# Kernel tuning notes

Hardware: AMD Instinct MI355X
Metric: run time of the kernel (lower is better)

## Reference

```python
import jax, jax.numpy as jnp
import numpy as np

B = 2048
IN = 1024
M = 256
P = M * (M + 1) // 2  # 32896 Cholesky params


def setup_inputs() -> dict:
    key = jax.random.key(0)
    k1, k2, k3 = jax.random.split(key, 3)
    x = jax.random.normal(k1, (B, IN), dtype=jnp.float32)
    # nn.Linear(input_size, P): weight [P, IN], bias [P]
    bound = 1.0 / np.sqrt(IN)
    W = jax.random.uniform(k2, (P, IN), dtype=jnp.float32, minval=-bound, maxval=bound)
    b = jax.random.uniform(k3, (P,), dtype=jnp.float32, minval=-bound, maxval=bound)
    return {"x": x, "W": W, "b": b}


def reference(x, W, b):
    # Linear projection to packed lower-triangular params [B, P]
    chol_params = x @ W.T + b
    # Row-major lower-triangular fill order matches the torch double loop:
    # (0,0),(1,0),(1,1),(2,0),...
    rows, cols = jnp.tril_indices(M)
    diag_mask = rows == cols  # [P]
    vals = jnp.where(diag_mask[None, :], jax.nn.relu(chol_params), chol_params)
    L = jnp.zeros((x.shape[0], M, M), dtype=chol_params.dtype)
    L = L.at[:, rows, cols].set(vals)
    # Batched L @ L^T -> positive semi-definite matrix [B, M, M]
    return jnp.einsum('bik,bjk->bij', L, L)
```

## Files before the change

kernel.cpp:

```cpp
#include <hip/hip_runtime.h>

#define B_DIM 2048
#define IN_DIM 1024
#define M_DIM 256
#define P_DIM 32896
#define RTP_B 40960
#define CRTP_BYTES (167772160)
#define WQ_BYTES   (33685504)
#define XQ_BYTES   (2097152)

typedef __attribute__((ext_vector_type(4)))  int   i32x4;
typedef __attribute__((ext_vector_type(4)))  float f32x4;
typedef __attribute__((ext_vector_type(8)))  short short8;

#define GLD16(gsrc, ldst) __builtin_amdgcn_global_load_lds(                    \
    (const __attribute__((address_space(1))) unsigned int*)(gsrc),             \
    (__attribute__((address_space(3))) unsigned int*)(ldst), 16, 0, 0)

__device__ __forceinline__ unsigned short f2bf(float f) {
    unsigned int u = __float_as_uint(f);
    u += 0x7FFFu + ((u >> 16) & 1u);
    return (unsigned short)(u >> 16);
}
__device__ __forceinline__ int rtp0(int r) {
    const int g = r >> 6;
    return 2048 * g * (g + 1) + (r & 63) * ((g + 1) << 6);
}
__device__ __forceinline__ int rtp_off(int r, int c) {
    return rtp0(r) + (((c >> 3) ^ (r & 7)) << 3) + (c & 7);
}

#define NW_BLK 8224
#define NX_BLK 512
#define NZ_BLK 2048
__global__ void prep_all(const float* __restrict__ X, const float* __restrict__ W,
                         signed char* __restrict__ Xq, signed char* __restrict__ Wq,
                         float* __restrict__ Sx, unsigned short* __restrict__ Crtp) {
    const int bid = blockIdx.x, tid = threadIdx.x;
    if (bid < NW_BLK) {
#pragma unroll
        for (int u = 0; u < 4; ++u) {
            const int i = bid * 1024 + u * 256 + tid;
            float4 v = reinterpret_cast<const float4*>(W)[i];
            const int q0 = (int)rintf(v.x * 4064.f), q1 = (int)rintf(v.y * 4064.f);
            const int q2 = (int)rintf(v.z * 4064.f), q3 = (int)rintf(v.w * 4064.f);
            reinterpret_cast<unsigned int*>(Wq)[i] =
                (q0 & 255) | ((q1 & 255) << 8) | ((q2 & 255) << 16) | ((unsigned)(q3 & 255) << 24);
        }
    } else if (bid < NW_BLK + NX_BLK) {
        const int wv  = tid >> 6, ln = tid & 63;
        const int row = (bid - NW_BLK) * 4 + wv;
        const float* xr = X + (size_t)row * IN_DIM + ln * 16;
        float f[16];
#pragma unroll
        for (int u = 0; u < 4; ++u) {
            float4 v = reinterpret_cast<const float4*>(xr)[u];
            f[u * 4 + 0] = v.x; f[u * 4 + 1] = v.y; f[u * 4 + 2] = v.z; f[u * 4 + 3] = v.w;
        }
        float m = 0.f;
#pragma unroll
        for (int e = 0; e < 16; ++e) m = fmaxf(m, fabsf(f[e]));
#pragma unroll
        for (int off = 1; off < 64; off <<= 1) m = fmaxf(m, __shfl_xor(m, off));
        const float inv = m > 1e-30f ? 127.f / m : 0.f;
        unsigned int w4[4];
#pragma unroll
        for (int u = 0; u < 4; ++u) {
            const int q0 = (int)rintf(f[u * 4 + 0] * inv), q1 = (int)rintf(f[u * 4 + 1] * inv);
            const int q2 = (int)rintf(f[u * 4 + 2] * inv), q3 = (int)rintf(f[u * 4 + 3] * inv);
            w4[u] = (q0 & 255) | ((q1 & 255) << 8) | ((q2 & 255) << 16) | ((unsigned)(q3 & 255) << 24);
        }
        reinterpret_cast<uint4*>(Xq + (size_t)row * IN_DIM)[ln] =
            make_uint4(w4[0], w4[1], w4[2], w4[3]);
        if (ln == 0) Sx[row] = m / (127.f * 4064.f);
    } else {
        const int b = bid - NW_BLK - NX_BLK;
        const int r = tid;
        const int g = r >> 6;
        const int nch = (g + 1) << 3;
        const int xm = r & 7;
        unsigned short* base = Crtp + (size_t)b * RTP_B + rtp0(r);
        const int pc = (r >> 3) ^ xm;
        for (int c = r + 1; (c >> 3) == (r >> 3); ++c) base[(pc << 3) + (c & 7)] = 0;
        const uint4 z = make_uint4(0u, 0u, 0u, 0u);
        for (int cc = (r >> 3) + 1; cc < nch; ++cc)
            *reinterpret_cast<uint4*>(&base[(cc ^ xm) << 3]) = z;
    }
}

__global__ __launch_bounds__(512) void gemm1_kernel(
    const signed char* __restrict__ Xq, const signed char* __restrict__ Wq,
    const float* __restrict__ bias, const float* __restrict__ Sx,
    unsigned short* __restrict__ Crtp)
{
    __shared__ __align__(16) unsigned char lds[3 * 24576];

    const int lin = blockIdx.x;
    const int x   = lin & 7;
    const int j   = lin >> 3;
    const int rtile = ((x & 1) << 2) + (j & 3);
    const int panel = (x >> 1) * 65 + (j >> 2);
    if (panel >= 257) return;
    const int row0 = rtile << 8;
    const int col0 = panel << 7;

    const int tid  = threadIdx.x;
    const int lane = tid & 63;
    const int wid  = tid >> 6;
    const int wr   = wid >> 1;
    const int wc   = wid & 1;
    const int lr16 = lane & 15;
    const int kq   = lane >> 4;

    const int srow = lane >> 2;
    const int sch  = lane & 3;
    const signed char* gA = Xq + (size_t)(row0 + (wid << 5) + srow) * IN_DIM + (sch << 4);
    const signed char* gB = Wq + (size_t)(col0 + (wid << 4) + srow) * IN_DIM + (sch << 4);

#define STAGE(kt, bufo)                                                          \
    {                                                                            \
        GLD16(gA + ((kt) << 6),                        &lds[(bufo) + (wid << 11)]); \
        GLD16(gA + (size_t)16 * IN_DIM + ((kt) << 6),  &lds[(bufo) + (wid << 11) + 1024]); \
        GLD16(gB + ((kt) << 6),                        &lds[(bufo) + 16384 + (wid << 10)]); \
    }

    i32x4 acc[4][4];
#pragma unroll
    for (int m = 0; m < 4; ++m)
#pragma unroll
        for (int n = 0; n < 4; ++n) acc[m][n] = (i32x4){0, 0, 0, 0};

    int o0 = 0, o1 = 24576, o2 = 49152;
    STAGE(0, o0);
    STAGE(1, o1);

    for (int it = 0; it < 16; ++it) {
        if (it < 15) asm volatile("s_waitcnt vmcnt(3)" ::: "memory");
        else         asm volatile("s_waitcnt vmcnt(0)" ::: "memory");
        __builtin_amdgcn_s_barrier();
        asm volatile("" ::: "memory");

        const int cb = o0;
        i32x4 av[4], bv[4];
#pragma unroll
        for (int m = 0; m < 4; ++m) {
            const int r = (wr << 6) + (m << 4) + lr16;
            av[m] = *reinterpret_cast<const i32x4*>(&lds[cb + (r << 6) + (kq << 4)]);
        }
#pragma unroll
        for (int n = 0; n < 4; ++n) {
            const int r = (wc << 6) + (n << 4) + lr16;
            bv[n] = *reinterpret_cast<const i32x4*>(&lds[cb + 16384 + (r << 6) + (kq << 4)]);
        }
        if (it < 14) STAGE(it + 2, o2);
        __builtin_amdgcn_s_setprio(1);
#pragma unroll
        for (int m = 0; m < 4; ++m)
#pragma unroll
            for (int n = 0; n < 4; ++n)
                acc[m][n] = __builtin_amdgcn_mfma_i32_16x16x64_i8(av[m], bv[n], acc[m][n], 0, 0, 0);
        __builtin_amdgcn_s_setprio(0);

        const int t = o0; o0 = o1; o1 = o2; o2 = t;
    }
#undef STAGE

    float sc[4][4];
#pragma unroll
    for (int m = 0; m < 4; ++m)
#pragma unroll
        for (int q = 0; q < 4; ++q)
            sc[m][q] = Sx[row0 + (wr << 6) + (m << 4) + (kq << 2) + q];

#pragma unroll
    for (int n = 0; n < 4; ++n) {
        const int p = col0 + (wc << 6) + (n << 4) + lr16;
        const float t = sqrtf((float)(8 * p + 1));
        const int rt = (int)((t - 1.0f) * 0.5f + 0.001f);
        const int ct = p - ((rt * (rt + 1)) >> 1);
        const int off = rtp_off(rt, ct);
        const bool diag = (ct == rt);
        const float bvs = bias[p];
#pragma unroll
        for (int m = 0; m < 4; ++m) {
#pragma unroll
            for (int q = 0; q < 4; ++q) {
                const int brow = row0 + (wr << 6) + (m << 4) + (kq << 2) + q;
                float v = (float)acc[m][n][q] * sc[m][q] + bvs;
                if (diag) v = fmaxf(v, 0.f);
                Crtp[(size_t)brow * RTP_B + off] = f2bf(v);
            }
        }
    }
}

__global__ __launch_bounds__(512) void syrk_kernel(
    const unsigned short* __restrict__ Crtp, float* __restrict__ O)
{
    __shared__ unsigned short Lt[RTP_B];
    const int tid  = threadIdx.x;
    const int lane = tid & 63;
    const int wid  = tid >> 6;
    const int b    = blockIdx.x;
    const unsigned short* Cb = Crtp + (size_t)b * RTP_B;

#pragma unroll
    for (int i = 0; i < 10; ++i) {
        const int g = wid * 10 + i;
        GLD16(Cb + g * 512 + (lane << 3), &Lt[g * 512]);
    }
    __syncthreads();

    const int lr16 = lane & 15;
    const int kc   = lane >> 4;
    float* Ob = O + (size_t)b * (M_DIM * M_DIM);

    const unsigned char LIST[8][3] = {
        {0x33, 0x00, 0x00},
        {0x22, 0x00, 0x00},
        {0x23, 0x01, 0x00},
        {0x32, 0x02, 0x00},
        {0x11, 0x12, 0x00},
        {0x21, 0x13, 0x00},
        {0x31, 0x10, 0x20},
        {0x30, 0x03, 0x00}};
    const int CNT[8] = {1, 2, 2, 2, 2, 2, 3, 2};
    const int cnt = CNT[wid];

    for (int tt = 0; tt < cnt; ++tt) {
        const int code = LIST[wid][tt];
        const int ti = code >> 4, tj = code & 15;

        int baseA[4], xA[4], baseB[4], xB[4];
#pragma unroll
        for (int m = 0; m < 4; ++m) {
            const int ia = (ti << 6) + (m << 4) + lr16;
            const int jb = (tj << 6) + (m << 4) + lr16;
            baseA[m] = rtp0(ia); xA[m] = ia & 7;
            baseB[m] = rtp0(jb); xB[m] = jb & 7;
        }
        f32x4 acc[4][4];
#pragma unroll
        for (int m = 0; m < 4; ++m)
#pragma unroll
            for (int n = 0; n < 4; ++n) acc[m][n] = (f32x4){0.f, 0.f, 0.f, 0.f};

        const int kmax = ti < tj ? ti : tj;
        for (int kt = 0; kt <= kmax; ++kt) {
#pragma unroll
            for (int s = 0; s < 2; ++s) {
                const int cidx = (kt << 3) + (s << 2) + kc;
                short8 a[4], bb[4];
#pragma unroll
                for (int m = 0; m < 4; ++m)
                    a[m] = *reinterpret_cast<const short8*>(&Lt[baseA[m] + ((cidx ^ xA[m]) << 3)]);
#pragma unroll
                for (int n = 0; n < 4; ++n)
                    bb[n] = *reinterpret_cast<const short8*>(&Lt[baseB[n] + ((cidx ^ xB[n]) << 3)]);
#pragma unroll
                for (int m = 0; m < 4; ++m)
#pragma unroll
                    for (int n = 0; n < 4; ++n)
                        acc[m][n] = __builtin_amdgcn_mfma_f32_16x16x32_bf16(a[m], bb[n], acc[m][n], 0, 0, 0);
            }
        }
#pragma unroll
        for (int m = 0; m < 4; ++m) {
            const int i0 = (ti << 6) + (m << 4) + (kc << 2);
#pragma unroll
            for (int n = 0; n < 4; ++n) {
                const int j = (tj << 6) + (n << 4) + lr16;
#pragma unroll
                for (int q = 0; q < 4; ++q)
                    __builtin_nontemporal_store(acc[m][n][q], &Ob[(size_t)(i0 + q) * M_DIM + j]);
            }
        }
    }
}

extern "C" void kernel_launch(void* const* d_in, const int* in_sizes, int n_in,
                              void* d_out, int out_size, void* d_ws, size_t ws_size,
                              hipStream_t stream)
{
    (void)in_sizes; (void)n_in; (void)out_size; (void)ws_size;
    const float* x    = (const float*)d_in[0];
    const float* W    = (const float*)d_in[1];
    const float* bias = (const float*)d_in[2];
    float* O = (float*)d_out;

    char* ws = (char*)d_ws;
    unsigned short* Crtp = (unsigned short*)ws;
    signed char*    Wq   = (signed char*)(ws + CRTP_BYTES);
    signed char*    Xq   = (signed char*)(ws + CRTP_BYTES + WQ_BYTES);
    float*          Sx   = (float*)(ws + CRTP_BYTES + WQ_BYTES + XQ_BYTES);

    prep_all<<<dim3(NW_BLK + NX_BLK + NZ_BLK), dim3(256), 0, stream>>>(
        x, W, Xq, Wq, Sx, Crtp);
    gemm1_kernel<<<dim3(2080), dim3(512), 0, stream>>>(Xq, Wq, bias, Sx, Crtp);
    syrk_kernel<<<dim3(B_DIM), dim3(512), 0, stream>>>(Crtp, O);
}
```

Before: 333.5 us.

## Split SYRK LDS load into two phases and compute early tiles during second load

The syrk kernel now loads the first 24 chunks of the packed L rows (covering rows 0-127) with a partial vmcnt wait and barrier. Two waves compute the tiles that depend only on those rows (00, 01, 10, 11) while the remaining chunks are still arriving. The other tiles are redistributed across waves after a second barrier. This overlaps global-to-LDS loading with MFMA work and the output stores, at the cost of less even per-wave work balance and reliance on hand-counted vmcnt values.

Measured after the change: 332.1 us. No clear change (-0.4%).

```diff
diff --git a/kernel.cpp b/kernel.cpp
--- a/kernel.cpp
+++ b/kernel.cpp
@@ -194,6 +194,56 @@
     }
 }
 
+__device__ __forceinline__ void syrk_tile(int code, const unsigned short* Lt,
+                                          float* __restrict__ Ob, int lr16, int kc)
+{
+    const int ti = code >> 4, tj = code & 15;
+    int baseA[4], xA[4], baseB[4], xB[4];
+#pragma unroll
+    for (int m = 0; m < 4; ++m) {
+        const int ia = (ti << 6) + (m << 4) + lr16;
+        const int jb = (tj << 6) + (m << 4) + lr16;
+        baseA[m] = rtp0(ia); xA[m] = ia & 7;
+        baseB[m] = rtp0(jb); xB[m] = jb & 7;
+    }
+    f32x4 acc[4][4];
+#pragma unroll
+    for (int m = 0; m < 4; ++m)
+#pragma unroll
+        for (int n = 0; n < 4; ++n) acc[m][n] = (f32x4){0.f, 0.f, 0.f, 0.f};
+
+    const int kmax = ti < tj ? ti : tj;
+    for (int kt = 0; kt <= kmax; ++kt) {
+#pragma unroll
+        for (int s = 0; s < 2; ++s) {
+            const int cidx = (kt << 3) + (s << 2) + kc;
+            short8 a[4], bb[4];
+#pragma unroll
+            for (int m = 0; m < 4; ++m)
+                a[m] = *reinterpret_cast<const short8*>(&Lt[baseA[m] + ((cidx ^ xA[m]) << 3)]);
+#pragma unroll
+            for (int n = 0; n < 4; ++n)
+                bb[n] = *reinterpret_cast<const short8*>(&Lt[baseB[n] + ((cidx ^ xB[n]) << 3)]);
+#pragma unroll
+            for (int m = 0; m < 4; ++m)
+#pragma unroll
+                for (int n = 0; n < 4; ++n)
+                    acc[m][n] = __builtin_amdgcn_mfma_f32_16x16x32_bf16(a[m], bb[n], acc[m][n], 0, 0, 0);
+        }
+    }
+#pragma unroll
+    for (int m = 0; m < 4; ++m) {
+        const int i0 = (ti << 6) + (m << 4) + (kc << 2);
+#pragma unroll
+        for (int n = 0; n < 4; ++n) {
+            const int j = (tj << 6) + (n << 4) + lr16;
+#pragma unroll
+            for (int q = 0; q < 4; ++q)
+                __builtin_nontemporal_store(acc[m][n][q], &Ob[(size_t)(i0 + q) * M_DIM + j]);
+        }
+    }
+}
+
 __global__ __launch_bounds__(512) void syrk_kernel(
     const unsigned short* __restrict__ Crtp, float* __restrict__ O)
 {
@@ -205,77 +255,47 @@
     const unsigned short* Cb = Crtp + (size_t)b * RTP_B;
 
 #pragma unroll
-    for (int i = 0; i < 10; ++i) {
-        const int g = wid * 10 + i;
+    for (int i = 0; i < 3; ++i) {
+        const int g = wid * 3 + i;
         GLD16(Cb + g * 512 + (lane << 3), &Lt[g * 512]);
     }
-    __syncthreads();
+#pragma unroll
+    for (int i = 0; i < 7; ++i) {
+        const int g = 24 + wid * 7 + i;
+        GLD16(Cb + g * 512 + (lane << 3), &Lt[g * 512]);
+    }
+    asm volatile("s_waitcnt vmcnt(7)" ::: "memory");
+    __builtin_amdgcn_s_barrier();
+    asm volatile("" ::: "memory");
 
     const int lr16 = lane & 15;
     const int kc   = lane >> 4;
     float* Ob = O + (size_t)b * (M_DIM * M_DIM);
 
-    const unsigned char LIST[8][3] = {
-        {0x33, 0x00, 0x00},
-        {0x22, 0x00, 0x00},
-        {0x23, 0x01, 0x00},
-        {0x32, 0x02, 0x00},
-        {0x11, 0x12, 0x00},
-        {0x21, 0x13, 0x00},
-        {0x31, 0x10, 0x20},
-        {0x30, 0x03, 0x00}};
-    const int CNT[8] = {1, 2, 2, 2, 2, 2, 3, 2};
-    const int cnt = CNT[wid];
-
-    for (int tt = 0; tt < cnt; ++tt) {
-        const int code = LIST[wid][tt];
-        const int ti = code >> 4, tj = code & 15;
-
-        int baseA[4], xA[4], baseB[4], xB[4];
-#pragma unroll
-        for (int m = 0; m < 4; ++m) {
-            const int ia = (ti << 6) + (m << 4) + lr16;
-            const int jb = (tj << 6) + (m << 4) + lr16;
-            baseA[m] = rtp0(ia); xA[m] = ia & 7;
-            baseB[m] = rtp0(jb); xB[m] = jb & 7;
-        }
-        f32x4 acc[4][4];
-#pragma unroll
-        for (int m = 0; m < 4; ++m)
-#pragma unroll
-            for (int n = 0; n < 4; ++n) acc[m][n] = (f32x4){0.f, 0.f, 0.f, 0.f};
-
-        const int kmax = ti < tj ? ti : tj;
-        for (int kt = 0; kt <= kmax; ++kt) {
-#pragma unroll
-            for (int s = 0; s < 2; ++s) {
-                const int cidx = (kt << 3) + (s << 2) + kc;
-                short8 a[4], bb[4];
-#pragma unroll
-                for (int m = 0; m < 4; ++m)
-                    a[m] = *reinterpret_cast<const short8*>(&Lt[baseA[m] + ((cidx ^ xA[m]) << 3)]);
-#pragma unroll
-                for (int n = 0; n < 4; ++n)
-                    bb[n] = *reinterpret_cast<const short8*>(&Lt[baseB[n] + ((cidx ^ xB[n]) << 3)]);
-#pragma unroll
-                for (int m = 0; m < 4; ++m)
-#pragma unroll
-                    for (int n = 0; n < 4; ++n)
-                        acc[m][n] = __builtin_amdgcn_mfma_f32_16x16x32_bf16(a[m], bb[n], acc[m][n], 0, 0, 0);
-            }
-        }
-#pragma unroll
-        for (int m = 0; m < 4; ++m) {
-            const int i0 = (ti << 6) + (m << 4) + (kc << 2);
-#pragma unroll
-            for (int n = 0; n < 4; ++n) {
-                const int j = (tj << 6) + (n << 4) + lr16;
-#pragma unroll
-                for (int q = 0; q < 4; ++q)
-                    __builtin_nontemporal_store(acc[m][n][q], &Ob[(size_t)(i0 + q) * M_DIM + j]);
-            }
-        }
-    }
+    const unsigned char L1[8][3] = {
+        {0,0,0},{0,0,0},{0,0,0},{0,0,0},{0,0,0},{0,0,0},
+        {0x11, 0, 0},
+        {0x00, 0x01, 0x10}};
+    const int C1[8] = {0, 0, 0, 0, 0, 0, 1, 3};
+    for (int tt = 0; tt < C1[wid]; ++tt)
+        syrk_tile(L1[wid][tt], Lt, Ob, lr16, kc);
+
+    asm volatile("s_waitcnt vmcnt(0)" ::: "memory");
+    __builtin_amdgcn_s_barrier();
+    asm volatile("" ::: "memory");
+
+    const unsigned char L2[8][2] = {
+        {0x33, 0x33},
+        {0x22, 0x02},
+        {0x23, 0x20},
+        {0x32, 0x30},
+        {0x12, 0x21},
+        {0x13, 0x31},
+        {0x03, 0x03},
+        {0x00, 0x00}};
+    const int C2[8] = {1, 2, 2, 2, 2, 2, 1, 0};
+    for (int tt = 0; tt < C2[wid]; ++tt)
+        syrk_tile(L2[wid][tt], Lt, Ob, lr16, kc);
 }
 
 extern "C" void kernel_launch(void* const* d_in, const int* in_sizes, int n_in,
```

## Enlarge int8 GEMM tiles to 256x256 and handle tail columns with separate blocks

Applied to the files above, without the earlier changes.

The main int8 GEMM moves from 256x128 tiles to 256x256 tiles, with eight waves each computing a 128x64 sub-tile, and LDS grows to three 32 KB buffers. The 128 leftover columns past 32768 are handled by extra blocks that load directly from global memory into MFMA without LDS. This doubles per-block data reuse and removes the swizzled 2080-block grid. The cost is more accumulator registers, lower occupancy from the larger LDS, and a slower unstaged tail path.

After: 351.2 us. 1.05x slower.

```diff
diff --git a/kernel.cpp b/kernel.cpp
--- a/kernel.cpp
+++ b/kernel.cpp
@@ -93,88 +93,31 @@
     const float* __restrict__ bias, const float* __restrict__ Sx,
     unsigned short* __restrict__ Crtp)
 {
-    __shared__ __align__(16) unsigned char lds[3 * 24576];
-
-    const int lin = blockIdx.x;
-    const int x   = lin & 7;
-    const int j   = lin >> 3;
-    const int rtile = ((x & 1) << 2) + (j & 3);
-    const int panel = (x >> 1) * 65 + (j >> 2);
-    if (panel >= 257) return;
-    const int row0 = rtile << 8;
-    const int col0 = panel << 7;
-
+    __shared__ __align__(16) unsigned char lds[3 * 32768];
+
+    const int bid  = blockIdx.x;
     const int tid  = threadIdx.x;
     const int lane = tid & 63;
     const int wid  = tid >> 6;
-    const int wr   = wid >> 1;
-    const int wc   = wid & 1;
     const int lr16 = lane & 15;
     const int kq   = lane >> 4;
 
-    const int srow = lane >> 2;
-    const int sch  = lane & 3;
-    const signed char* gA = Xq + (size_t)(row0 + (wid << 5) + srow) * IN_DIM + (sch << 4);
-    const signed char* gB = Wq + (size_t)(col0 + (wid << 4) + srow) * IN_DIM + (sch << 4);
-
-#define STAGE(kt, bufo)                                                          \
-    {                                                                            \
-        GLD16(gA + ((kt) << 6),                        &lds[(bufo) + (wid << 11)]); \
-        GLD16(gA + (size_t)16 * IN_DIM + ((kt) << 6),  &lds[(bufo) + (wid << 11) + 1024]); \
-        GLD16(gB + ((kt) << 6),                        &lds[(bufo) + 16384 + (wid << 10)]); \
-    }
-
-    i32x4 acc[4][4];
-#pragma unroll
-    for (int m = 0; m < 4; ++m)
-#pragma unroll
-        for (int n = 0; n < 4; ++n) acc[m][n] = (i32x4){0, 0, 0, 0};
-
-    int o0 = 0, o1 = 24576, o2 = 49152;
-    STAGE(0, o0);
-    STAGE(1, o1);
-
-    for (int it = 0; it < 16; ++it) {
-        if (it < 15) asm volatile("s_waitcnt vmcnt(3)" ::: "memory");
-        else         asm volatile("s_waitcnt vmcnt(0)" ::: "memory");
-        __builtin_amdgcn_s_barrier();
-        asm volatile("" ::: "memory");
-
-        const int cb = o0;
-        i32x4 av[4], bv[4];
-#pragma unroll
-        for (int m = 0; m < 4; ++m) {
-            const int r = (wr << 6) + (m << 4) + lr16;
-            av[m] = *reinterpret_cast<const i32x4*>(&lds[cb + (r << 6) + (kq << 4)]);
-        }
-#pragma unroll
-        for (int n = 0; n < 4; ++n) {
-            const int r = (wc << 6) + (n << 4) + lr16;
-            bv[n] = *reinterpret_cast<const i32x4*>(&lds[cb + 16384 + (r << 6) + (kq << 4)]);
-        }
-        if (it < 14) STAGE(it + 2, o2);
-        __builtin_amdgcn_s_setprio(1);
-#pragma unroll
-        for (int m = 0; m < 4; ++m)
-#pragma unroll
-            for (int n = 0; n < 4; ++n)
-                acc[m][n] = __builtin_amdgcn_mfma_i32_16x16x64_i8(av[m], bv[n], acc[m][n], 0, 0, 0);
-        __builtin_amdgcn_s_setprio(0);
-
-        const int t = o0; o0 = o1; o1 = o2; o2 = t;
-    }
-#undef STAGE
-
-    float sc[4][4];
-#pragma unroll
-    for (int m = 0; m < 4; ++m)
-#pragma unroll
-        for (int q = 0; q < 4; ++q)
-            sc[m][q] = Sx[row0 + (wr << 6) + (m << 4) + (kq << 2) + q];
-
-#pragma unroll
-    for (int n = 0; n < 4; ++n) {
-        const int p = col0 + (wc << 6) + (n << 4) + lr16;
+    if (bid >= 1024) {
+        const int tb = bid - 1024;
+        const int r0 = tb << 5;
+        i32x4 acc0 = (i32x4){0,0,0,0}, acc1 = (i32x4){0,0,0,0};
+        const signed char* pa0 = Xq + (size_t)(r0 + lr16) * IN_DIM + (kq << 4);
+        const signed char* pa1 = pa0 + 16 * IN_DIM;
+        const int p = 32768 + (wid << 4) + lr16;
+        const signed char* pb = Wq + (size_t)p * IN_DIM + (kq << 4);
+#pragma unroll 4
+        for (int s = 0; s < 16; ++s) {
+            i32x4 a0 = *reinterpret_cast<const i32x4*>(pa0 + (s << 6));
+            i32x4 a1 = *reinterpret_cast<const i32x4*>(pa1 + (s << 6));
+            i32x4 b0 = *reinterpret_cast<const i32x4*>(pb + (s << 6));
+            acc0 = __builtin_amdgcn_mfma_i32_16x16x64_i8(a0, b0, acc0, 0, 0, 0);
+            acc1 = __builtin_amdgcn_mfma_i32_16x16x64_i8(a1, b0, acc1, 0, 0, 0);
+        }
         const float t = sqrtf((float)(8 * p + 1));
         const int rt = (int)((t - 1.0f) * 0.5f + 0.001f);
         const int ct = p - ((rt * (rt + 1)) >> 1);
@@ -182,10 +125,101 @@
         const bool diag = (ct == rt);
         const float bvs = bias[p];
 #pragma unroll
-        for (int m = 0; m < 4; ++m) {
+        for (int m = 0; m < 2; ++m) {
+            const i32x4 a = m ? acc1 : acc0;
 #pragma unroll
             for (int q = 0; q < 4; ++q) {
-                const int brow = row0 + (wr << 6) + (m << 4) + (kq << 2) + q;
+                const int brow = r0 + (m << 4) + (kq << 2) + q;
+                float v = (float)a[q] * Sx[brow] + bvs;
+                if (diag) v = fmaxf(v, 0.f);
+                Crtp[(size_t)brow * RTP_B + off] = f2bf(v);
+            }
+        }
+        return;
+    }
+
+    const int row0 = (bid & 7) << 8;
+    const int col0 = (bid >> 3) << 8;
+    const int wr   = wid >> 2;
+    const int wn   = wid & 3;
+
+    const int srow = lane >> 2;
+    const int sch  = lane & 3;
+    const signed char* gA0 = Xq + (size_t)(row0 + (wid << 5) + srow) * IN_DIM + (sch << 4);
+    const signed char* gA1 = gA0 + (size_t)16 * IN_DIM;
+    const signed char* gB0 = Wq + (size_t)(col0 + (wid << 5) + srow) * IN_DIM + (sch << 4);
+    const signed char* gB1 = gB0 + (size_t)16 * IN_DIM;
+
+#define STAGE(kt, bufo)                                                        \
+    {                                                                          \
+        GLD16(gA0 + ((kt) << 6), &lds[(bufo) + (wid << 11)]);                  \
+        GLD16(gA1 + ((kt) << 6), &lds[(bufo) + (wid << 11) + 1024]);           \
+        GLD16(gB0 + ((kt) << 6), &lds[(bufo) + 16384 + (wid << 11)]);          \
+        GLD16(gB1 + ((kt) << 6), &lds[(bufo) + 16384 + (wid << 11) + 1024]);   \
+    }
+
+    i32x4 acc[8][4];
+#pragma unroll
+    for (int m = 0; m < 8; ++m)
+#pragma unroll
+        for (int n = 0; n < 4; ++n) acc[m][n] = (i32x4){0, 0, 0, 0};
+
+    int o0 = 0, o1 = 32768, o2 = 65536;
+    STAGE(0, o0);
+    STAGE(1, o1);
+
+    for (int it = 0; it < 16; ++it) {
+        if (it < 15) asm volatile("s_waitcnt vmcnt(4)" ::: "memory");
+        else         asm volatile("s_waitcnt vmcnt(0)" ::: "memory");
+        __builtin_amdgcn_s_barrier();
+        asm volatile("" ::: "memory");
+
+        const int cb = o0;
+        i32x4 av[8], bv[4];
+#pragma unroll
+        for (int m = 0; m < 8; ++m) {
+            const int r = (wr << 7) + (m << 4) + lr16;
+            av[m] = *reinterpret_cast<const i32x4*>(&lds[cb + (r << 6) + (kq << 4)]);
+        }
+#pragma unroll
+        for (int n = 0; n < 4; ++n) {
+            const int r = (wn << 6) + (n << 4) + lr16;
+            bv[n] = *reinterpret_cast<const i32x4*>(&lds[cb + 16384 + (r << 6) + (kq << 4)]);
+        }
+        if (it < 14) STAGE(it + 2, o2);
+        __builtin_amdgcn_s_setprio(1);
+#pragma unroll
+        for (int m = 0; m < 8; ++m)
+#pragma unroll
+            for (int n = 0; n < 4; ++n)
+                acc[m][n] = __builtin_amdgcn_mfma_i32_16x16x64_i8(av[m], bv[n], acc[m][n], 0, 0, 0);
+        __builtin_amdgcn_s_setprio(0);
+
+        const int t = o0; o0 = o1; o1 = o2; o2 = t;
+    }
+#undef STAGE
+
+    float sc[8][4];
+#pragma unroll
+    for (int m = 0; m < 8; ++m)
+#pragma unroll
+        for (int q = 0; q < 4; ++q)
+            sc[m][q] = Sx[row0 + (wr << 7) + (m << 4) + (kq << 2) + q];
+
+#pragma unroll
+    for (int n = 0; n < 4; ++n) {
+        const int p = col0 + (wn << 6) + (n << 4) + lr16;
+        const float t = sqrtf((float)(8 * p + 1));
+        const int rt = (int)((t - 1.0f) * 0.5f + 0.001f);
+        const int ct = p - ((rt * (rt + 1)) >> 1);
+        const int off = rtp_off(rt, ct);
+        const bool diag = (ct == rt);
+        const float bvs = bias[p];
+#pragma unroll
+        for (int m = 0; m < 8; ++m) {
+#pragma unroll
+            for (int q = 0; q < 4; ++q) {
+                const int brow = row0 + (wr << 7) + (m << 4) + (kq << 2) + q;
                 float v = (float)acc[m][n][q] * sc[m][q] + bvs;
                 if (diag) v = fmaxf(v, 0.f);
                 Crtp[(size_t)brow * RTP_B + off] = f2bf(v);
@@ -296,6 +330,6 @@
 
     prep_all<<<dim3(NW_BLK + NX_BLK + NZ_BLK), dim3(256), 0, stream>>>(
         x, W, Xq, Wq, Sx, Crtp);
-    gemm1_kernel<<<dim3(2080), dim3(512), 0, stream>>>(Xq, Wq, bias, Sx, Crtp);
+    gemm1_kernel<<<dim3(1088), dim3(512), 0, stream>>>(Xq, Wq, bias, Sx, Crtp);
     syrk_kernel<<<dim3(B_DIM), dim3(512), 0, stream>>>(Crtp, O);
 }
```
